# Performance work log

Hardware: AMD Instinct MI355X
Metric: run time of the kernel (lower is better)

The kernel has to match this reference:

```python
import jax, jax.numpy as jnp
import numpy as np

EPS = 1e-5

def _layernorm(x, gamma, beta):
    # normalize over last (channel) axis, per point
    mu = jnp.mean(x, axis=-1, keepdims=True)
    var = jnp.mean(jnp.square(x - mu), axis=-1, keepdims=True)
    return (x - mu) * jax.lax.rsqrt(var + EPS) * gamma + beta

def setup_inputs() -> dict:
    key = jax.random.key(0)
    ks = jax.random.split(key, 12)
    B, N, C, F = 32, 4096, 3, 1024
    points = jax.random.normal(ks[0], (B, N, C), dtype=jnp.float32)
    mask = jax.random.randint(ks[1], (B, 1, N), 0, 2, dtype=jnp.int32)
    s = 0.05
    return {
        "points": points,
        "mask": mask,
        "w1": jax.random.normal(ks[2], (128, C), dtype=jnp.float32) * s,      # conv1 (no bias)
        "g1": jnp.ones((128,), jnp.float32),                                   # norm1 gamma
        "be1": jnp.zeros((128,), jnp.float32),                                 # norm1 beta
        "w2": jax.random.normal(ks[3], (256, 128), dtype=jnp.float32) * s,     # conv2
        "b2": jax.random.normal(ks[4], (256,), dtype=jnp.float32) * s,
        "w3": jax.random.normal(ks[5], (512, 512), dtype=jnp.float32) * s,     # conv3 (no bias)
        "g2": jnp.ones((512,), jnp.float32),                                   # norm2 gamma
        "be2": jnp.zeros((512,), jnp.float32),                                 # norm2 beta
        "w4": jax.random.normal(ks[6], (F, 512), dtype=jnp.float32) * s,       # conv4
        "b4": jax.random.normal(ks[7], (F,), dtype=jnp.float32) * s,
    }

def reference(points, mask, w1, g1, be1, w2, b2, w3, g2, be2, w4, b4):
    # points: [B, N, C]; mask: [B, 1, N]
    vis = (mask[:, 0, :] != 0).astype(points.dtype)[..., None]  # [B, N, 1]
    # conv1 (1x1, no bias) as point-wise matmul
    h0 = jnp.einsum('bnc,kc->bnk', points, w1)                  # [B, N, 128]
    # masked LayerNorm: LN is per-point over channels, so compute densely and zero invisible points
    h1 = _layernorm(h0, g1, be1) * vis
    h2 = jax.nn.relu(h1)
    h3 = jnp.einsum('bnk,ok->bno', h2, w2) + b2                 # [B, N, 256]
    gmax = jnp.max(h3, axis=1, keepdims=True)                   # [B, 1, 256]
    dist = jnp.concatenate([jnp.broadcast_to(gmax, h3.shape), h3], axis=-1)  # [B, N, 512]
    h4 = jnp.einsum('bno,po->bnp', dist, w3)                    # [B, N, 512]
    h5 = _layernorm(h4, g2, be2) * vis
    h6 = jax.nn.relu(h5)
    h7 = jnp.einsum('bnp,fp->bnf', h6, w4) + b4                 # [B, N, F]
    return jnp.max(h7, axis=1)                                  # [B, F]
```

## Files before the change

kernel.cpp:

```cpp
#include <hip/hip_runtime.h>
#include <stdint.h>

#define LN_EPS 1e-5f

static __device__ __forceinline__ unsigned short f2bf_bits(float f) {
  union { float f; unsigned u; } v; v.f = f;
  unsigned r = v.u + 0x7FFFu + ((v.u >> 16) & 1u);
  return (unsigned short)(r >> 16);
}
static __device__ __forceinline__ float bf2f(unsigned short h) {
  union { unsigned u; float f; } v; v.u = ((unsigned)h) << 16;
  return v.f;
}

typedef __bf16 bf16x8 __attribute__((ext_vector_type(8)));
typedef float floatx4 __attribute__((ext_vector_type(4)));

typedef __attribute__((address_space(1))) unsigned int* gas_ptr;
typedef __attribute__((address_space(3))) unsigned int* las_ptr;
static __device__ __forceinline__ void async_cp16(const void* g, void* l) {
  __builtin_amdgcn_global_load_lds((gas_ptr)g, (las_ptr)l, 16, 0, 0);
}

__global__ __launch_bounds__(256) void perm_kernel(
    const int* __restrict__ mask, int* __restrict__ newrow, int* __restrict__ cnt) {
  const int b = blockIdx.x, t = threadIdx.x;
  const int base = b * 4096 + t * 16;
  int v[16]; int s = 0;
#pragma unroll
  for (int i = 0; i < 16; ++i) { v[i] = (mask[base + i] != 0); s += v[i]; }
  const int lane = t & 63, wv = t >> 6;
  int scan = s;
  for (int o = 1; o < 64; o <<= 1) { int x = __shfl_up(scan, o); if (lane >= o) scan += x; }
  __shared__ int wsum[4], woff[4], stotal;
  if (lane == 63) wsum[wv] = scan;
  __syncthreads();
  if (t == 0) { int a = 0; for (int k = 0; k < 4; ++k) { woff[k] = a; a += wsum[k]; } stotal = a; cnt[b] = a; }
  __syncthreads();
  const int excl = scan - s + woff[wv];
  const int total = stotal;
  int run = 0;
#pragma unroll
  for (int i = 0; i < 16; ++i) {
    const int pos = t * 16 + i;
    const int visBefore = excl + run;
    newrow[b * 4096 + pos] = v[i] ? visBefore : total + (pos - visBefore);
    run += v[i];
  }
}

__global__ __launch_bounds__(256) void conv1_ln_kernel(
    const float* __restrict__ points,
    const float* __restrict__ w1, const float* __restrict__ g1,
    const float* __restrict__ be1, unsigned short* __restrict__ h2,
    const int* __restrict__ newrow, const int* __restrict__ cnt,
    const float* __restrict__ w2, const float* __restrict__ b2,
    const float* __restrict__ w3, const float* __restrict__ w4,
    unsigned short* __restrict__ w2b, unsigned short* __restrict__ w4b,
    unsigned short* __restrict__ w23b, float* __restrict__ vecb) {
  if (blockIdx.x >= 32768) {
    const int bb = blockIdx.x - 32768;
    if (bb < 2176) {
      int idx = bb * 256 + threadIdx.x;
      if (idx < 32768) w2b[idx] = f2bf_bits(w2[idx]);
      else w4b[idx - 32768] = f2bf_bits(w4[idx - 32768]);
    } else {
      const int tid = threadIdx.x;
      const int p = (bb - 2176) * 2 + (tid >> 7);
      const int c = tid & 127;
      const float* w3r = w3 + (size_t)p * 512 + 256;
      float s = 0.f;
      for (int k = 0; k < 256; ++k) s += w3r[k] * w2[k * 128 + c];
      w23b[p * 128 + c] = f2bf_bits(s);
      if (c == 0) {
        float vb = 0.f;
        for (int k = 0; k < 256; ++k) vb += w3r[k] * b2[k];
        vecb[p] = vb;
      }
    }
    return;
  }
  const int lane = threadIdx.x & 63;
  const int wv = threadIdx.x >> 6;
  const size_t p = (size_t)blockIdx.x * 4 + wv;
  const int dest = newrow[p];
  const int cntb = cnt[p >> 12];
  const int ceilv = (cntb + 127) & ~127;
  if (dest >= ceilv) return;
  const bool vis = (dest < cntb);
  const float x0 = points[p * 3 + 0];
  const float x1 = points[p * 3 + 1];
  const float x2 = points[p * 3 + 2];
  const int c0 = lane * 2, c1 = c0 + 1;
  float h00 = w1[c0 * 3] * x0 + w1[c0 * 3 + 1] * x1 + w1[c0 * 3 + 2] * x2;
  float h01 = w1[c1 * 3] * x0 + w1[c1 * 3 + 1] * x1 + w1[c1 * 3 + 2] * x2;
  float s = h00 + h01;
  for (int o = 32; o; o >>= 1) s += __shfl_xor(s, o);
  const float mu = s * (1.f / 128.f);
  const float d0 = h00 - mu, d1 = h01 - mu;
  float q = d0 * d0 + d1 * d1;
  for (int o = 32; o; o >>= 1) q += __shfl_xor(q, o);
  const float rs = rsqrtf(q * (1.f / 128.f) + LN_EPS);
  const float y0 = vis ? fmaxf(d0 * rs * g1[c0] + be1[c0], 0.f) : 0.f;
  const float y1 = vis ? fmaxf(d1 * rs * g1[c1] + be1[c1], 0.f) : 0.f;
  union { unsigned u; unsigned short s2[2]; } pk;
  pk.s2[0] = f2bf_bits(y0);
  pk.s2[1] = f2bf_bits(y1);
  const size_t prow = (p & ~(size_t)4095) + (size_t)dest;
  ((unsigned*)h2)[prow * 64 + lane] = pk.u;
}

__global__ __launch_bounds__(256) void gemm23_fused(
    const unsigned short* __restrict__ A,
    const unsigned short* __restrict__ w2b, const unsigned short* __restrict__ w23b,
    unsigned short* __restrict__ h46, float* __restrict__ pg,
    const float* __restrict__ b2, const float* __restrict__ vecb,
    const int* __restrict__ cnt, int M) {
  __shared__ __align__(16) char smA[2][128 * 64];
  __shared__ __align__(16) char smB[2][128 * 64];
  __shared__ float lmax[2][128];

  const int tid = threadIdx.x;
  const int lane = tid & 63;
  const int w = tid >> 6;
  const int wm = w >> 1, wn = w & 1;

  const int gid = blockIdx.x;
  const int xcd = gid & 7;
  const int slot = gid >> 3;
  const int rowsPerXcd = (M >> 7) >> 3;
  const int rowTile = xcd * rowsPerXcd + slot / 6;
  const int colTile = slot % 6;
  const bool isPG = (colTile < 2);
  const int colBase = isPG ? colTile * 128 : (colTile - 2) * 128;
  const size_t rowBase = (size_t)rowTile * 128;
  const unsigned short* Bw = isPG ? w2b : w23b;

  const int cntb = cnt[rowBase >> 12];
  const int rb = (int)(rowBase & 4095);
  if (rb >= cntb) {
    if (isPG) {
      if (tid < 128) pg[(size_t)rowTile * 256 + colBase + tid] = b2[colBase + tid];
    }
    return;
  }

  floatx4 acc[4][4];
  const floatx4 zero = {0.f, 0.f, 0.f, 0.f};
#pragma unroll
  for (int i = 0; i < 4; ++i)
#pragma unroll
    for (int j = 0; j < 4; ++j) acc[i][j] = zero;

  const int rSub = lane >> 2;
  const int cb16 = (lane & 3) * 16;
  const size_t Kb = 256;
  const char* gA = (const char*)A + (rowBase + (size_t)(w * 32 + rSub)) * Kb + cb16;
  const char* gB = (const char*)Bw + ((size_t)colBase + (size_t)(w * 32 + rSub)) * Kb + cb16;
  char* lA0 = smA[0] + w * 2048;
  char* lA1 = smA[1] + w * 2048;
  char* lB0 = smB[0] + w * 2048;
  char* lB1 = smB[1] + w * 2048;
  const size_t skip16 = 16 * Kb;

  const int fm = lane & 15, fq = lane >> 4;
  const int fOff = fm * 64 + fq * 16;
  const char* pa0 = smA[0] + wm * 64 * 64 + fOff;
  const char* pa1 = smA[1] + wm * 64 * 64 + fOff;
  const char* pb0 = smB[0] + wn * 64 * 64 + fOff;
  const char* pb1 = smB[1] + wn * 64 * 64 + fOff;

  for (int k0 = 0; k0 < 128; k0 += 64) {
    async_cp16(gA, lA0);
    async_cp16(gA + skip16, lA0 + 1024);
    async_cp16(gA + 64, lA1);
    async_cp16(gA + 64 + skip16, lA1 + 1024);
    async_cp16(gB, lB0);
    async_cp16(gB + skip16, lB0 + 1024);
    async_cp16(gB + 64, lB1);
    async_cp16(gB + 64 + skip16, lB1 + 1024);
    gA += 128; gB += 128;
    __syncthreads();
    bf16x8 af0[4], bg0[4], af1[4], bg1[4];
#pragma unroll
    for (int i = 0; i < 4; ++i) af0[i] = *(const bf16x8*)(pa0 + i * 16 * 64);
#pragma unroll
    for (int j = 0; j < 4; ++j) bg0[j] = *(const bf16x8*)(pb0 + j * 16 * 64);
#pragma unroll
    for (int i = 0; i < 4; ++i)
#pragma unroll
      for (int j = 0; j < 4; ++j)
        acc[i][j] = __builtin_amdgcn_mfma_f32_16x16x32_bf16(af0[i], bg0[j], acc[i][j], 0, 0, 0);
#pragma unroll
    for (int i = 0; i < 4; ++i) af1[i] = *(const bf16x8*)(pa1 + i * 16 * 64);
#pragma unroll
    for (int j = 0; j < 4; ++j) bg1[j] = *(const bf16x8*)(pb1 + j * 16 * 64);
#pragma unroll
    for (int i = 0; i < 4; ++i)
#pragma unroll
      for (int j = 0; j < 4; ++j)
        acc[i][j] = __builtin_amdgcn_mfma_f32_16x16x32_bf16(af1[i], bg1[j], acc[i][j], 0, 0, 0);
    __syncthreads();
  }

  if (isPG) {
    float m4[4] = {-1e30f, -1e30f, -1e30f, -1e30f};
#pragma unroll
    for (int j = 0; j < 4; ++j) {
      const float ex = b2[colBase + wn * 64 + j * 16 + fm];
#pragma unroll
      for (int i = 0; i < 4; ++i)
#pragma unroll
        for (int r = 0; r < 4; ++r) m4[j] = fmaxf(m4[j], acc[i][j][r] + ex);
      m4[j] = fmaxf(m4[j], __shfl_xor(m4[j], 16));
      m4[j] = fmaxf(m4[j], __shfl_xor(m4[j], 32));
    }
    const float sel = (fq == 0) ? m4[0] : (fq == 1) ? m4[1] : (fq == 2) ? m4[2] : m4[3];
    lmax[wm][wn * 64 + fq * 16 + fm] = sel;
    __syncthreads();
    if (tid < 128) {
      const float v = fmaxf(lmax[0][tid], lmax[1][tid]);
      pg[(size_t)rowTile * 256 + colBase + tid] = v;
    }
  } else {
#pragma unroll
    for (int j = 0; j < 4; ++j) {
      const int col = colBase + wn * 64 + j * 16 + fm;
      const float ex = vecb[col];
#pragma unroll
      for (int i = 0; i < 4; ++i) {
        const size_t row0 = rowBase + wm * 64 + i * 16 + fq * 4;
#pragma unroll
        for (int r = 0; r < 4; ++r) {
          h46[(row0 + r) * 512 + col] = f2bf_bits(acc[i][j][r] + ex);
        }
      }
    }
  }
}

#define G4_BAR() __builtin_amdgcn_s_barrier()
#define G4_LGKM0() asm volatile("s_waitcnt lgkmcnt(0)" ::: "memory")
#define G4_LGKM8() asm volatile("s_waitcnt lgkmcnt(8)" ::: "memory")
#define G4_VM2() asm volatile("s_waitcnt vmcnt(2)" ::: "memory")
#define G4_VM0() asm volatile("s_waitcnt vmcnt(0)" ::: "memory")
#define G4_PRIO1() __builtin_amdgcn_s_setprio(1)
#define G4_PRIO0() __builtin_amdgcn_s_setprio(0)

#define G4_STG(bufi, h4, kt) do { \
  const char* _s = (((h4) < 2) ? srcA : srcB) + (size_t)((h4) & 1) * (128 * 1024) + (size_t)(kt) * 128; \
  char* _d = stDst + (bufi) * 65536 + ((h4) >> 1) * 32768 + ((h4) & 1) * 16384; \
  async_cp16(_s, _d); \
  async_cp16(_s + 64 * 1024, _d + 8192); \
} while (0)

#define G4_LDA(bufi, mh) do { \
  const char* _p = rdA + (bufi) * 65536 + (mh) * 8192; \
  af[0][0] = *(const bf16x8*)(_p + c0);        af[0][1] = *(const bf16x8*)(_p + c1); \
  af[1][0] = *(const bf16x8*)(_p + 2048 + c0); af[1][1] = *(const bf16x8*)(_p + 2048 + c1); \
  af[2][0] = *(const bf16x8*)(_p + 4096 + c0); af[2][1] = *(const bf16x8*)(_p + 4096 + c1); \
  af[3][0] = *(const bf16x8*)(_p + 6144 + c0); af[3][1] = *(const bf16x8*)(_p + 6144 + c1); \
} while (0)

#define G4_LDB(bufi, nh, bgx) do { \
  const char* _p = rdB + (bufi) * 65536 + (nh) * 4096; \
  bgx[0][0] = *(const bf16x8*)(_p + c0);        bgx[0][1] = *(const bf16x8*)(_p + c1); \
  bgx[1][0] = *(const bf16x8*)(_p + 2048 + c0); bgx[1][1] = *(const bf16x8*)(_p + 2048 + c1); \
} while (0)

#define G4_QUAD(mh, nh, bgx) do { \
  _Pragma("unroll") \
  for (int _m = 0; _m < 4; ++_m) { \
    _Pragma("unroll") \
    for (int _n = 0; _n < 2; ++_n) { \
      acc[(mh) * 4 + _m][(nh) * 2 + _n] = __builtin_amdgcn_mfma_f32_16x16x32_bf16( \
          af[_m][0], bgx[_n][0], acc[(mh) * 4 + _m][(nh) * 2 + _n], 0, 0, 0); \
      acc[(mh) * 4 + _m][(nh) * 2 + _n] = __builtin_amdgcn_mfma_f32_16x16x32_bf16( \
          af[_m][1], bgx[_n][1], acc[(mh) * 4 + _m][(nh) * 2 + _n], 0, 0, 0); \
    } \
  } \
} while (0)

__global__ __launch_bounds__(512, 2) void gemm4_8ph(
    const unsigned short* __restrict__ A, const unsigned short* __restrict__ Bw,
    float* __restrict__ outp2, const int* __restrict__ cnt) {
  extern __shared__ char sm[];

  const int tid = threadIdx.x;
  const int lane = tid & 63;
  const int w = tid >> 6;
  const int wm = w >> 2, wn = w & 3;

  const int gid = blockIdx.x;
  const int xcd = gid & 7;
  const int slot = gid >> 3;
  const int rowTile = xcd * 64 + (slot >> 2);
  const int colTile = slot & 3;
  const size_t rowBase = (size_t)rowTile * 256;
  const int colBase = colTile * 256;

  const int cntb = cnt[rowBase >> 12];
  const int rb = (int)(rowBase & 4095);
  if (rb >= cntb) {
    if (tid < 256) outp2[(size_t)rowTile * 1024 + colBase + tid] = 0.f;
    return;
  }

  const int rr = tid >> 3;
  const int csw = ((tid & 7) ^ (rr & 7)) << 4;
  const char* srcA = (const char*)A + (rowBase + (size_t)rr) * 1024 + csw;
  const char* srcB = (const char*)Bw + ((size_t)colBase + (size_t)rr) * 1024 + csw;
  char* stDst = sm + w * 1024;

  const int fr = lane & 15, fq = lane >> 4;
  const int c0 = (fq * 16) ^ ((lane & 7) << 4);
  const int c1 = ((fq * 16) | 64) ^ ((lane & 7) << 4);
  const char* rdA = sm + (wm * 128 + fr) * 128;
  const char* rdB = sm + 32768 + (wn * 64 + fr) * 128;

  floatx4 acc[8][4];
  const floatx4 zero = {0.f, 0.f, 0.f, 0.f};
#pragma unroll
  for (int i = 0; i < 8; ++i)
#pragma unroll
    for (int j = 0; j < 4; ++j) acc[i][j] = zero;

  bf16x8 af[4][2], bg0[2][2], bg1[2][2];

  G4_STG(0, 0, 0); G4_STG(0, 1, 0); G4_STG(0, 2, 0); G4_STG(0, 3, 0);
  G4_STG(1, 0, 1);
  G4_VM2(); G4_BAR();

  for (int it = 0; it < 3; ++it) {
    const int tO = 2 * it + 1, tE2 = 2 * it + 2, tO2 = 2 * it + 3;
    G4_LDA(0, 0); G4_LDB(0, 0, bg0); G4_STG(1, 1, tO); G4_LGKM8(); G4_BAR(); G4_LGKM0();
    G4_PRIO1(); G4_QUAD(0, 0, bg0); G4_PRIO0(); G4_BAR();
    G4_LDB(0, 1, bg1); G4_STG(1, 2, tO); G4_BAR(); G4_LGKM0();
    G4_PRIO1(); G4_QUAD(0, 1, bg1); G4_PRIO0(); G4_BAR();
    G4_LDA(0, 1); G4_STG(1, 3, tO); G4_BAR(); G4_LGKM0();
    G4_PRIO1(); G4_QUAD(1, 1, bg1); G4_PRIO0(); G4_BAR();
    G4_STG(0, 0, tE2); G4_VM2(); G4_BAR();
    G4_PRIO1(); G4_QUAD(1, 0, bg0); G4_PRIO0(); G4_BAR();
    G4_LDA(1, 0); G4_LDB(1, 0, bg0); G4_STG(0, 1, tE2); G4_LGKM8(); G4_BAR(); G4_LGKM0();
    G4_PRIO1(); G4_QUAD(0, 0, bg0); G4_PRIO0(); G4_BAR();
    G4_LDB(1, 1, bg1); G4_STG(0, 2, tE2); G4_BAR(); G4_LGKM0();
    G4_PRIO1(); G4_QUAD(0, 1, bg1); G4_PRIO0(); G4_BAR();
    G4_LDA(1, 1); G4_STG(0, 3, tE2); G4_BAR(); G4_LGKM0();
    G4_PRIO1(); G4_QUAD(1, 1, bg1); G4_PRIO0(); G4_BAR();
    G4_STG(1, 0, tO2); G4_VM2(); G4_BAR();
    G4_PRIO1(); G4_QUAD(1, 0, bg0); G4_PRIO0(); G4_BAR();
  }

  G4_LDA(0, 0); G4_LDB(0, 0, bg0); G4_STG(1, 1, 7); G4_LGKM8(); G4_BAR(); G4_LGKM0();
  G4_PRIO1(); G4_QUAD(0, 0, bg0); G4_PRIO0(); G4_BAR();
  G4_LDB(0, 1, bg1); G4_STG(1, 2, 7); G4_BAR(); G4_LGKM0();
  G4_PRIO1(); G4_QUAD(0, 1, bg1); G4_PRIO0(); G4_BAR();
  G4_LDA(0, 1); G4_STG(1, 3, 7); G4_BAR(); G4_LGKM0();
  G4_PRIO1(); G4_QUAD(1, 1, bg1); G4_PRIO0(); G4_BAR();
  G4_VM0(); G4_BAR();
  G4_PRIO1(); G4_QUAD(1, 0, bg0); G4_PRIO0(); G4_BAR();
  G4_LDA(1, 0); G4_LDB(1, 0, bg0); G4_BAR(); G4_LGKM0();
  G4_PRIO1(); G4_QUAD(0, 0, bg0); G4_PRIO0(); G4_BAR();
  G4_LDB(1, 1, bg1); G4_BAR(); G4_LGKM0();
  G4_PRIO1(); G4_QUAD(0, 1, bg1); G4_PRIO0(); G4_BAR();
  G4_LDA(1, 1); G4_BAR(); G4_LGKM0();
  G4_PRIO1(); G4_QUAD(1, 1, bg1); G4_PRIO0(); G4_BAR();
  G4_PRIO1(); G4_QUAD(1, 0, bg0); G4_PRIO0(); G4_BAR();

  float* smf = (float*)sm;
  float mv[4];
#pragma unroll
  for (int nj = 0; nj < 4; ++nj) {
    float m = -1e30f;
#pragma unroll
    for (int mi = 0; mi < 8; ++mi)
#pragma unroll
      for (int r = 0; r < 4; ++r) m = fmaxf(m, acc[mi][nj][r]);
    m = fmaxf(m, __shfl_xor(m, 16));
    m = fmaxf(m, __shfl_xor(m, 32));
    mv[nj] = m;
  }
  const float sel = (fq == 0) ? mv[0] : (fq == 1) ? mv[1] : (fq == 2) ? mv[2] : mv[3];
  smf[wm * 256 + wn * 64 + fq * 16 + fr] = sel;
  __syncthreads();
  if (tid < 256) {
    outp2[(size_t)rowTile * 1024 + colBase + tid] = fmaxf(smf[tid], smf[256 + tid]);
  }
}

__global__ __launch_bounds__(256) void gmax_cvec_kernel(
    const float* __restrict__ pg, const float* __restrict__ w3,
    float* __restrict__ cvec) {
  __shared__ float gm[256];
  const int b = blockIdx.x >> 2, quarter = blockIdx.x & 3;
  const int t = threadIdx.x;
  float m = -1e30f;
  for (int s = 0; s < 32; ++s) m = fmaxf(m, pg[((size_t)b * 32 + s) * 256 + t]);
  gm[t] = m;
  __syncthreads();
  const int lane = t & 63, wv = t >> 6;
  const float g0 = gm[lane * 4 + 0];
  const float g1 = gm[lane * 4 + 1];
  const float g2v = gm[lane * 4 + 2];
  const float g3 = gm[lane * 4 + 3];
  for (int pp = 0; pp < 32; ++pp) {
    const int p = quarter * 128 + wv * 32 + pp;
    const float4 wr = *(const float4*)(w3 + (size_t)p * 512 + lane * 4);
    float s = wr.x * g0 + wr.y * g1 + wr.z * g2v + wr.w * g3;
    for (int o = 32; o; o >>= 1) s += __shfl_xor(s, o);
    if (lane == 0) cvec[b * 512 + p] = s;
  }
}

__global__ __launch_bounds__(256) void ln2_kernel(
    unsigned short* __restrict__ h46, const int* __restrict__ cnt,
    const float* __restrict__ cvec,
    const float* __restrict__ g2, const float* __restrict__ be2) {
  const int lane = threadIdx.x & 63;
  const int wv = threadIdx.x >> 6;
  const size_t p = (size_t)blockIdx.x * 4 + wv;
  const int cb = cnt[p >> 12];
  const int pin = (int)(p & 4095);
  const int ceilv = (cb + 255) & ~255;
  if (pin >= ceilv) return;
  unsigned short* row = h46 + p * 512;
  const int c0 = lane * 8;
  if (pin >= cb) {
    const uint4 z = {0, 0, 0, 0};
    *(uint4*)(row + c0) = z;
    return;
  }
  const int b = (int)(p >> 12);
  union { uint4 v; unsigned short s[8]; } in;
  in.v = *(const uint4*)(row + c0);
  float cv[8];
  *(float4*)(cv) = *(const float4*)(cvec + b * 512 + c0);
  *(float4*)(cv + 4) = *(const float4*)(cvec + b * 512 + c0 + 4);
  float f[8];
  float s = 0.f;
#pragma unroll
  for (int k = 0; k < 8; ++k) { f[k] = bf2f(in.s[k]) + cv[k]; s += f[k]; }
  for (int o = 32; o; o >>= 1) s += __shfl_xor(s, o);
  const float mu = s * (1.f / 512.f);
  float q = 0.f;
#pragma unroll
  for (int k = 0; k < 8; ++k) { const float d = f[k] - mu; q += d * d; }
  for (int o = 32; o; o >>= 1) q += __shfl_xor(q, o);
  const float rs = rsqrtf(q * (1.f / 512.f) + LN_EPS);
  union { uint4 v; unsigned short s[8]; } outv;
#pragma unroll
  for (int k = 0; k < 8; ++k) {
    const float y = fmaxf((f[k] - mu) * rs * g2[c0 + k] + be2[c0 + k], 0.f);
    outv.s[k] = f2bf_bits(y);
  }
  *(uint4*)(row + c0) = outv.v;
}

__global__ __launch_bounds__(256) void final_kernel(
    const float* __restrict__ pmax, const float* __restrict__ b4,
    float* __restrict__ out) {
  const int idx = blockIdx.x * 256 + threadIdx.x;
  const int b = idx >> 10, f = idx & 1023;
  float m = -1e30f;
  for (int r = 0; r < 16; ++r) m = fmaxf(m, pmax[((size_t)(b * 16 + r)) * 1024 + f]);
  out[idx] = m + b4[f];
}

extern "C" void kernel_launch(void* const* d_in, const int* in_sizes, int n_in,
                              void* d_out, int out_size, void* d_ws, size_t ws_size,
                              hipStream_t stream) {
  const float* points = (const float*)d_in[0];
  const int* mask = (const int*)d_in[1];
  const float* w1 = (const float*)d_in[2];
  const float* g1 = (const float*)d_in[3];
  const float* be1 = (const float*)d_in[4];
  const float* w2 = (const float*)d_in[5];
  const float* b2 = (const float*)d_in[6];
  const float* w3 = (const float*)d_in[7];
  const float* g2 = (const float*)d_in[8];
  const float* be2 = (const float*)d_in[9];
  const float* w4 = (const float*)d_in[10];
  const float* b4 = (const float*)d_in[11];
  float* out = (float*)d_out;
  char* ws = (char*)d_ws;

  const size_t OFF_H46 = 0;
  const size_t OFF_H2 = 134217728;
  const size_t OFF_W2B = OFF_H2 + 33554432;
  const size_t OFF_W4B = OFF_W2B + 65536;
  const size_t OFF_W23B = OFF_W4B + 1048576;
  const size_t OFF_VECB = OFF_W23B + 131072;
  const size_t OFF_PG = OFF_VECB + 2048;
  const size_t OFF_CVEC = OFF_PG + 1048576;
  const size_t OFF_PMAX = OFF_CVEC + 65536;
  const size_t OFF_CNT = OFF_PMAX + 4194304;
  const size_t OFF_NEWROW = OFF_CNT + 4096;

  unsigned short* h2 = (unsigned short*)(ws + OFF_H2);
  unsigned short* h46 = (unsigned short*)(ws + OFF_H46);
  unsigned short* w2b = (unsigned short*)(ws + OFF_W2B);
  unsigned short* w4b = (unsigned short*)(ws + OFF_W4B);
  unsigned short* w23b = (unsigned short*)(ws + OFF_W23B);
  float* vecb = (float*)(ws + OFF_VECB);
  float* pg = (float*)(ws + OFF_PG);
  float* cvecp = (float*)(ws + OFF_CVEC);
  float* pmaxp = (float*)(ws + OFF_PMAX);
  int* cntp = (int*)(ws + OFF_CNT);
  int* newrow = (int*)(ws + OFF_NEWROW);

  static bool s_attr_done = false;
  if (!s_attr_done) {
    hipFuncSetAttribute((const void*)gemm4_8ph,
                        hipFuncAttributeMaxDynamicSharedMemorySize, 131072);
    s_attr_done = true;
  }

  perm_kernel<<<32, 256, 0, stream>>>(mask, newrow, cntp);
  conv1_ln_kernel<<<32768 + 2176 + 256, 256, 0, stream>>>(
      points, w1, g1, be1, h2, newrow, cntp, w2, b2, w3, w4, w2b, w4b, w23b, vecb);
  gemm23_fused<<<6144, 256, 0, stream>>>(h2, w2b, w23b, h46, pg, b2, vecb, cntp, 131072);
  gmax_cvec_kernel<<<128, 256, 0, stream>>>(pg, w3, cvecp);
  ln2_kernel<<<32768, 256, 0, stream>>>(h46, cntp, cvecp, g2, be2);
  gemm4_8ph<<<2048, 512, 131072, stream>>>(h46, w4b, pmaxp, cntp);
  final_kernel<<<128, 256, 0, stream>>>(pmaxp, b4, out);
}
```

Baseline: 268.1 us.

## Compact tile work lists so GEMM and LN2 blocks map only to visible tiles

Adds a per-batch prefix scan over visible-point counts that builds compacted lists of occupied 128-row and 256-row tiles. gemm23, ln2 and gemm4 map block indices directly onto these lists, so the leading blocks all do real work and the surplus blocks exit at once. Before, empty tiles were spread across the grid and each wrote placeholder partial results. The reduction kernels now loop only over occupied tiles and seed their max with the empty-point value (b2 or zero) when a batch has invisible points. This removes wasted scheduling and placeholder writes, but drops the XCD-aware tile mapping, which may hurt L2 locality.

```diff
diff --git a/kernel.cpp b/kernel.cpp
--- a/kernel.cpp
+++ b/kernel.cpp
@@ -57,14 +57,16 @@
     const float* __restrict__ w2, const float* __restrict__ b2,
     const float* __restrict__ w3, const float* __restrict__ w4,
     unsigned short* __restrict__ w2b, unsigned short* __restrict__ w4b,
-    unsigned short* __restrict__ w23b, float* __restrict__ vecb) {
+    unsigned short* __restrict__ w23b, float* __restrict__ vecb,
+    int* __restrict__ hdr, unsigned short* __restrict__ tl128,
+    unsigned short* __restrict__ tl256) {
   if (blockIdx.x >= 32768) {
     const int bb = blockIdx.x - 32768;
     if (bb < 2176) {
       int idx = bb * 256 + threadIdx.x;
       if (idx < 32768) w2b[idx] = f2bf_bits(w2[idx]);
       else w4b[idx - 32768] = f2bf_bits(w4[idx - 32768]);
-    } else {
+    } else if (bb < 2176 + 256) {
       const int tid = threadIdx.x;
       const int p = (bb - 2176) * 2 + (tid >> 7);
       const int c = tid & 127;
@@ -76,6 +78,24 @@
         float vb = 0.f;
         for (int k = 0; k < 256; ++k) vb += w3r[k] * b2[k];
         vecb[p] = vb;
+      }
+    } else {
+      const int lane = threadIdx.x;
+      if (lane < 64) {
+        const int c = (lane < 32) ? cnt[lane] : 0;
+        const int n128 = (c + 127) >> 7;
+        const int n256 = (c + 255) >> 8;
+        int s128 = n128, s256 = n256;
+        for (int o = 1; o < 64; o <<= 1) {
+          int x = __shfl_up(s128, o); if (lane >= o) s128 += x;
+          int y = __shfl_up(s256, o); if (lane >= o) s256 += y;
+        }
+        if (lane == 31) { hdr[0] = s128; hdr[1] = s256; }
+        if (lane < 32) {
+          const int e128 = s128 - n128, e256 = s256 - n256;
+          for (int j = 0; j < n128; ++j) tl128[e128 + j] = (unsigned short)(lane * 32 + j);
+          for (int j = 0; j < n256; ++j) tl256[e256 + j] = (unsigned short)(lane * 16 + j);
+        }
       }
     }
     return;
@@ -115,35 +135,26 @@
     const unsigned short* __restrict__ w2b, const unsigned short* __restrict__ w23b,
     unsigned short* __restrict__ h46, float* __restrict__ pg,
     const float* __restrict__ b2, const float* __restrict__ vecb,
-    const int* __restrict__ cnt, int M) {
+    const int* __restrict__ hdr, const unsigned short* __restrict__ tl128) {
   __shared__ __align__(16) char smA[2][128 * 64];
   __shared__ __align__(16) char smB[2][128 * 64];
   __shared__ float lmax[2][128];
+
+  const int nW = hdr[0] * 6;
+  if (blockIdx.x >= nW) return;
+  const int t6 = blockIdx.x / 6;
+  const int colTile = blockIdx.x - t6 * 6;
+  const int rowTile = tl128[t6];
 
   const int tid = threadIdx.x;
   const int lane = tid & 63;
   const int w = tid >> 6;
   const int wm = w >> 1, wn = w & 1;
 
-  const int gid = blockIdx.x;
-  const int xcd = gid & 7;
-  const int slot = gid >> 3;
-  const int rowsPerXcd = (M >> 7) >> 3;
-  const int rowTile = xcd * rowsPerXcd + slot / 6;
-  const int colTile = slot % 6;
   const bool isPG = (colTile < 2);
   const int colBase = isPG ? colTile * 128 : (colTile - 2) * 128;
   const size_t rowBase = (size_t)rowTile * 128;
   const unsigned short* Bw = isPG ? w2b : w23b;
-
-  const int cntb = cnt[rowBase >> 12];
-  const int rb = (int)(rowBase & 4095);
-  if (rb >= cntb) {
-    if (isPG) {
-      if (tid < 128) pg[(size_t)rowTile * 256 + colBase + tid] = b2[colBase + tid];
-    }
-    return;
-  }
 
   floatx4 acc[4][4];
   const floatx4 zero = {0.f, 0.f, 0.f, 0.f};
@@ -283,28 +294,22 @@
 
 __global__ __launch_bounds__(512, 2) void gemm4_8ph(
     const unsigned short* __restrict__ A, const unsigned short* __restrict__ Bw,
-    float* __restrict__ outp2, const int* __restrict__ cnt) {
+    float* __restrict__ outp2, const int* __restrict__ hdr,
+    const unsigned short* __restrict__ tl256) {
   extern __shared__ char sm[];
+
+  const int nW = hdr[1] * 4;
+  if (blockIdx.x >= nW) return;
+  const int rowTile = tl256[blockIdx.x >> 2];
+  const int colTile = blockIdx.x & 3;
 
   const int tid = threadIdx.x;
   const int lane = tid & 63;
   const int w = tid >> 6;
   const int wm = w >> 2, wn = w & 3;
 
-  const int gid = blockIdx.x;
-  const int xcd = gid & 7;
-  const int slot = gid >> 3;
-  const int rowTile = xcd * 64 + (slot >> 2);
-  const int colTile = slot & 3;
   const size_t rowBase = (size_t)rowTile * 256;
   const int colBase = colTile * 256;
-
-  const int cntb = cnt[rowBase >> 12];
-  const int rb = (int)(rowBase & 4095);
-  if (rb >= cntb) {
-    if (tid < 256) outp2[(size_t)rowTile * 1024 + colBase + tid] = 0.f;
-    return;
-  }
 
   const int rr = tid >> 3;
   const int csw = ((tid & 7) ^ (rr & 7)) << 4;
@@ -390,12 +395,15 @@
 
 __global__ __launch_bounds__(256) void gmax_cvec_kernel(
     const float* __restrict__ pg, const float* __restrict__ w3,
-    float* __restrict__ cvec) {
+    float* __restrict__ cvec, const int* __restrict__ cnt,
+    const float* __restrict__ b2) {
   __shared__ float gm[256];
   const int b = blockIdx.x >> 2, quarter = blockIdx.x & 3;
   const int t = threadIdx.x;
-  float m = -1e30f;
-  for (int s = 0; s < 32; ++s) m = fmaxf(m, pg[((size_t)b * 32 + s) * 256 + t]);
+  const int c = cnt[b];
+  const int nt = (c + 127) >> 7;
+  float m = (c < 4096) ? b2[t] : -1e30f;
+  for (int s = 0; s < nt; ++s) m = fmaxf(m, pg[((size_t)b * 32 + s) * 256 + t]);
   gm[t] = m;
   __syncthreads();
   const int lane = t & 63, wv = t >> 6;
@@ -415,14 +423,17 @@
 __global__ __launch_bounds__(256) void ln2_kernel(
     unsigned short* __restrict__ h46, const int* __restrict__ cnt,
     const float* __restrict__ cvec,
-    const float* __restrict__ g2, const float* __restrict__ be2) {
+    const float* __restrict__ g2, const float* __restrict__ be2,
+    const int* __restrict__ hdr, const unsigned short* __restrict__ tl256) {
+  const int nW = hdr[1] * 64;
+  if (blockIdx.x >= nW) return;
+  const int rowTile = tl256[blockIdx.x >> 6];
   const int lane = threadIdx.x & 63;
   const int wv = threadIdx.x >> 6;
-  const size_t p = (size_t)blockIdx.x * 4 + wv;
-  const int cb = cnt[p >> 12];
+  const size_t p = (size_t)rowTile * 256 + ((blockIdx.x & 63) * 4 + wv);
+  const int b = rowTile >> 4;
+  const int cb = cnt[b];
   const int pin = (int)(p & 4095);
-  const int ceilv = (cb + 255) & ~255;
-  if (pin >= ceilv) return;
   unsigned short* row = h46 + p * 512;
   const int c0 = lane * 8;
   if (pin >= cb) {
@@ -430,7 +441,6 @@
     *(uint4*)(row + c0) = z;
     return;
   }
-  const int b = (int)(p >> 12);
   union { uint4 v; unsigned short s[8]; } in;
   in.v = *(const uint4*)(row + c0);
   float cv[8];
@@ -458,11 +468,13 @@
 
 __global__ __launch_bounds__(256) void final_kernel(
     const float* __restrict__ pmax, const float* __restrict__ b4,
-    float* __restrict__ out) {
+    float* __restrict__ out, const int* __restrict__ cnt) {
   const int idx = blockIdx.x * 256 + threadIdx.x;
   const int b = idx >> 10, f = idx & 1023;
-  float m = -1e30f;
-  for (int r = 0; r < 16; ++r) m = fmaxf(m, pmax[((size_t)(b * 16 + r)) * 1024 + f]);
+  const int c = cnt[b];
+  const int nt = (c + 255) >> 8;
+  float m = (c < 4096) ? 0.f : -1e30f;
+  for (int r = 0; r < nt; ++r) m = fmaxf(m, pmax[((size_t)(b * 16 + r)) * 1024 + f]);
   out[idx] = m + b4[f];
 }
 
@@ -495,6 +507,9 @@
   const size_t OFF_PMAX = OFF_CVEC + 65536;
   const size_t OFF_CNT = OFF_PMAX + 4194304;
   const size_t OFF_NEWROW = OFF_CNT + 4096;
+  const size_t OFF_HDR = OFF_NEWROW + 524288;
+  const size_t OFF_TL128 = OFF_HDR + 64;
+  const size_t OFF_TL256 = OFF_TL128 + 2048;
 
   unsigned short* h2 = (unsigned short*)(ws + OFF_H2);
   unsigned short* h46 = (unsigned short*)(ws + OFF_H46);
@@ -507,6 +522,9 @@
   float* pmaxp = (float*)(ws + OFF_PMAX);
   int* cntp = (int*)(ws + OFF_CNT);
   int* newrow = (int*)(ws + OFF_NEWROW);
+  int* hdr = (int*)(ws + OFF_HDR);
+  unsigned short* tl128 = (unsigned short*)(ws + OFF_TL128);
+  unsigned short* tl256 = (unsigned short*)(ws + OFF_TL256);
 
   static bool s_attr_done = false;
   if (!s_attr_done) {
@@ -516,11 +534,12 @@
   }
 
   perm_kernel<<<32, 256, 0, stream>>>(mask, newrow, cntp);
-  conv1_ln_kernel<<<32768 + 2176 + 256, 256, 0, stream>>>(
-      points, w1, g1, be1, h2, newrow, cntp, w2, b2, w3, w4, w2b, w4b, w23b, vecb);
-  gemm23_fused<<<6144, 256, 0, stream>>>(h2, w2b, w23b, h46, pg, b2, vecb, cntp, 131072);
-  gmax_cvec_kernel<<<128, 256, 0, stream>>>(pg, w3, cvecp);
-  ln2_kernel<<<32768, 256, 0, stream>>>(h46, cntp, cvecp, g2, be2);
-  gemm4_8ph<<<2048, 512, 131072, stream>>>(h46, w4b, pmaxp, cntp);
-  final_kernel<<<128, 256, 0, stream>>>(pmaxp, b4, out);
-}
+  conv1_ln_kernel<<<32768 + 2176 + 256 + 1, 256, 0, stream>>>(
+      points, w1, g1, be1, h2, newrow, cntp, w2, b2, w3, w4, w2b, w4b, w23b, vecb,
+      hdr, tl128, tl256);
+  gemm23_fused<<<6144, 256, 0, stream>>>(h2, w2b, w23b, h46, pg, b2, vecb, hdr, tl128);
+  gmax_cvec_kernel<<<128, 256, 0, stream>>>(pg, w3, cvecp, cntp, b2);
+  ln2_kernel<<<32768, 256, 0, stream>>>(h46, cntp, cvecp, g2, be2, hdr, tl256);
+  gemm4_8ph<<<2048, 512, 131072, stream>>>(h46, w4b, pmaxp, hdr, tl256);
+  final_kernel<<<128, 256, 0, stream>>>(pmaxp, b4, out, cntp);
+}
```

Result: slower. 284.6 us (+6.2%).

## Reuse A tile across two column tiles and skip empty-tile writes

Applied to the files above, without the earlier changes.

The fused GEMM2/GEMM23 kernel now loads each block's full 128x128 A tile into shared memory once and reuses it across two 128-column output phases, halving the grid and the A reloads. Fully masked row tiles now return early without writing placeholder values. The downstream reductions (gmax_cvec and final) read the valid count and iterate only over populated tiles, adding the bias or zero contribution for masked points analytically. In exchange, each block does twice the work, shared memory use grows, and correctness now depends on the count-based tile bounds matching the early-exit logic.

```diff
diff --git a/kernel.cpp b/kernel.cpp
--- a/kernel.cpp
+++ b/kernel.cpp
@@ -115,124 +115,125 @@
     const unsigned short* __restrict__ w2b, const unsigned short* __restrict__ w23b,
     unsigned short* __restrict__ h46, float* __restrict__ pg,
     const float* __restrict__ b2, const float* __restrict__ vecb,
-    const int* __restrict__ cnt, int M) {
-  __shared__ __align__(16) char smA[2][128 * 64];
+    const int* __restrict__ cnt) {
+  __shared__ __align__(16) char smA[4][128 * 64];
   __shared__ __align__(16) char smB[2][128 * 64];
   __shared__ float lmax[2][128];
+
+  const int gid = blockIdx.x;
+  const int xcd = gid & 7;
+  const int slot = gid >> 3;
+  const int rowTile = xcd * 128 + slot / 3;
+  const int pair = slot - (slot / 3) * 3;
+  const size_t rowBase = (size_t)rowTile * 128;
+
+  const int cntb = cnt[rowBase >> 12];
+  const int rb = (int)(rowBase & 4095);
+  if (rb >= cntb) return;
 
   const int tid = threadIdx.x;
   const int lane = tid & 63;
   const int w = tid >> 6;
   const int wm = w >> 1, wn = w & 1;
 
-  const int gid = blockIdx.x;
-  const int xcd = gid & 7;
-  const int slot = gid >> 3;
-  const int rowsPerXcd = (M >> 7) >> 3;
-  const int rowTile = xcd * rowsPerXcd + slot / 6;
-  const int colTile = slot % 6;
-  const bool isPG = (colTile < 2);
-  const int colBase = isPG ? colTile * 128 : (colTile - 2) * 128;
-  const size_t rowBase = (size_t)rowTile * 128;
+  const bool isPG = (pair == 0);
   const unsigned short* Bw = isPG ? w2b : w23b;
-
-  const int cntb = cnt[rowBase >> 12];
-  const int rb = (int)(rowBase & 4095);
-  if (rb >= cntb) {
-    if (isPG) {
-      if (tid < 128) pg[(size_t)rowTile * 256 + colBase + tid] = b2[colBase + tid];
-    }
-    return;
-  }
-
-  floatx4 acc[4][4];
-  const floatx4 zero = {0.f, 0.f, 0.f, 0.f};
-#pragma unroll
-  for (int i = 0; i < 4; ++i)
-#pragma unroll
-    for (int j = 0; j < 4; ++j) acc[i][j] = zero;
 
   const int rSub = lane >> 2;
   const int cb16 = (lane & 3) * 16;
-  const size_t Kb = 256;
-  const char* gA = (const char*)A + (rowBase + (size_t)(w * 32 + rSub)) * Kb + cb16;
-  const char* gB = (const char*)Bw + ((size_t)colBase + (size_t)(w * 32 + rSub)) * Kb + cb16;
-  char* lA0 = smA[0] + w * 2048;
-  char* lA1 = smA[1] + w * 2048;
+  const size_t skip16 = 16 * 256;
+
+  const char* gA = (const char*)A + (rowBase + (size_t)(w * 32 + rSub)) * 256 + cb16;
+#pragma unroll
+  for (int q = 0; q < 4; ++q) {
+    async_cp16(gA + q * 64, smA[q] + w * 2048);
+    async_cp16(gA + q * 64 + skip16, smA[q] + w * 2048 + 1024);
+  }
+
   char* lB0 = smB[0] + w * 2048;
   char* lB1 = smB[1] + w * 2048;
-  const size_t skip16 = 16 * Kb;
 
   const int fm = lane & 15, fq = lane >> 4;
   const int fOff = fm * 64 + fq * 16;
-  const char* pa0 = smA[0] + wm * 64 * 64 + fOff;
-  const char* pa1 = smA[1] + wm * 64 * 64 + fOff;
   const char* pb0 = smB[0] + wn * 64 * 64 + fOff;
   const char* pb1 = smB[1] + wn * 64 * 64 + fOff;
 
-  for (int k0 = 0; k0 < 128; k0 += 64) {
-    async_cp16(gA, lA0);
-    async_cp16(gA + skip16, lA0 + 1024);
-    async_cp16(gA + 64, lA1);
-    async_cp16(gA + 64 + skip16, lA1 + 1024);
-    async_cp16(gB, lB0);
-    async_cp16(gB + skip16, lB0 + 1024);
-    async_cp16(gB + 64, lB1);
-    async_cp16(gB + 64 + skip16, lB1 + 1024);
-    gA += 128; gB += 128;
-    __syncthreads();
-    bf16x8 af0[4], bg0[4], af1[4], bg1[4];
-#pragma unroll
-    for (int i = 0; i < 4; ++i) af0[i] = *(const bf16x8*)(pa0 + i * 16 * 64);
-#pragma unroll
-    for (int j = 0; j < 4; ++j) bg0[j] = *(const bf16x8*)(pb0 + j * 16 * 64);
+  const floatx4 zero = {0.f, 0.f, 0.f, 0.f};
+
+  for (int ph = 0; ph < 2; ++ph) {
+    const int bRow = isPG ? ph * 128 : ((pair - 1) * 256 + ph * 128);
+    floatx4 acc[4][4];
 #pragma unroll
     for (int i = 0; i < 4; ++i)
 #pragma unroll
-      for (int j = 0; j < 4; ++j)
-        acc[i][j] = __builtin_amdgcn_mfma_f32_16x16x32_bf16(af0[i], bg0[j], acc[i][j], 0, 0, 0);
-#pragma unroll
-    for (int i = 0; i < 4; ++i) af1[i] = *(const bf16x8*)(pa1 + i * 16 * 64);
-#pragma unroll
-    for (int j = 0; j < 4; ++j) bg1[j] = *(const bf16x8*)(pb1 + j * 16 * 64);
-#pragma unroll
-    for (int i = 0; i < 4; ++i)
-#pragma unroll
-      for (int j = 0; j < 4; ++j)
-        acc[i][j] = __builtin_amdgcn_mfma_f32_16x16x32_bf16(af1[i], bg1[j], acc[i][j], 0, 0, 0);
-    __syncthreads();
-  }
-
-  if (isPG) {
-    float m4[4] = {-1e30f, -1e30f, -1e30f, -1e30f};
-#pragma unroll
-    for (int j = 0; j < 4; ++j) {
-      const float ex = b2[colBase + wn * 64 + j * 16 + fm];
+      for (int j = 0; j < 4; ++j) acc[i][j] = zero;
+
+    const char* gB = (const char*)Bw + ((size_t)(bRow + w * 32 + rSub)) * 256 + cb16;
+
+    for (int k0i = 0; k0i < 2; ++k0i) {
+      async_cp16(gB, lB0);
+      async_cp16(gB + skip16, lB0 + 1024);
+      async_cp16(gB + 64, lB1);
+      async_cp16(gB + 64 + skip16, lB1 + 1024);
+      gB += 128;
+      __syncthreads();
+      const char* pa0 = smA[2 * k0i] + wm * 64 * 64 + fOff;
+      const char* pa1 = smA[2 * k0i + 1] + wm * 64 * 64 + fOff;
+      bf16x8 af0[4], bg0[4], af1[4], bg1[4];
+#pragma unroll
+      for (int i = 0; i < 4; ++i) af0[i] = *(const bf16x8*)(pa0 + i * 16 * 64);
+#pragma unroll
+      for (int j = 0; j < 4; ++j) bg0[j] = *(const bf16x8*)(pb0 + j * 16 * 64);
 #pragma unroll
       for (int i = 0; i < 4; ++i)
 #pragma unroll
-        for (int r = 0; r < 4; ++r) m4[j] = fmaxf(m4[j], acc[i][j][r] + ex);
-      m4[j] = fmaxf(m4[j], __shfl_xor(m4[j], 16));
-      m4[j] = fmaxf(m4[j], __shfl_xor(m4[j], 32));
+        for (int j = 0; j < 4; ++j)
+          acc[i][j] = __builtin_amdgcn_mfma_f32_16x16x32_bf16(af0[i], bg0[j], acc[i][j], 0, 0, 0);
+#pragma unroll
+      for (int i = 0; i < 4; ++i) af1[i] = *(const bf16x8*)(pa1 + i * 16 * 64);
+#pragma unroll
+      for (int j = 0; j < 4; ++j) bg1[j] = *(const bf16x8*)(pb1 + j * 16 * 64);
+#pragma unroll
+      for (int i = 0; i < 4; ++i)
+#pragma unroll
+        for (int j = 0; j < 4; ++j)
+          acc[i][j] = __builtin_amdgcn_mfma_f32_16x16x32_bf16(af1[i], bg1[j], acc[i][j], 0, 0, 0);
+      __syncthreads();
     }
-    const float sel = (fq == 0) ? m4[0] : (fq == 1) ? m4[1] : (fq == 2) ? m4[2] : m4[3];
-    lmax[wm][wn * 64 + fq * 16 + fm] = sel;
-    __syncthreads();
-    if (tid < 128) {
-      const float v = fmaxf(lmax[0][tid], lmax[1][tid]);
-      pg[(size_t)rowTile * 256 + colBase + tid] = v;
-    }
-  } else {
-#pragma unroll
-    for (int j = 0; j < 4; ++j) {
-      const int col = colBase + wn * 64 + j * 16 + fm;
-      const float ex = vecb[col];
-#pragma unroll
-      for (int i = 0; i < 4; ++i) {
-        const size_t row0 = rowBase + wm * 64 + i * 16 + fq * 4;
-#pragma unroll
-        for (int r = 0; r < 4; ++r) {
-          h46[(row0 + r) * 512 + col] = f2bf_bits(acc[i][j][r] + ex);
+
+    if (isPG) {
+      const int colBase = ph * 128;
+      float m4[4] = {-1e30f, -1e30f, -1e30f, -1e30f};
+#pragma unroll
+      for (int j = 0; j < 4; ++j) {
+        const float ex = b2[colBase + wn * 64 + j * 16 + fm];
+#pragma unroll
+        for (int i = 0; i < 4; ++i)
+#pragma unroll
+          for (int r = 0; r < 4; ++r) m4[j] = fmaxf(m4[j], acc[i][j][r] + ex);
+        m4[j] = fmaxf(m4[j], __shfl_xor(m4[j], 16));
+        m4[j] = fmaxf(m4[j], __shfl_xor(m4[j], 32));
+      }
+      const float sel = (fq == 0) ? m4[0] : (fq == 1) ? m4[1] : (fq == 2) ? m4[2] : m4[3];
+      lmax[wm][wn * 64 + fq * 16 + fm] = sel;
+      __syncthreads();
+      if (tid < 128) {
+        const float v = fmaxf(lmax[0][tid], lmax[1][tid]);
+        pg[(size_t)rowTile * 256 + colBase + tid] = v;
+      }
+    } else {
+      const int colBase = (pair - 1) * 256 + ph * 128;
+#pragma unroll
+      for (int j = 0; j < 4; ++j) {
+        const int col = colBase + wn * 64 + j * 16 + fm;
+        const float ex = vecb[col];
+#pragma unroll
+        for (int i = 0; i < 4; ++i) {
+          const size_t row0 = rowBase + wm * 64 + i * 16 + fq * 4;
+#pragma unroll
+          for (int r = 0; r < 4; ++r) {
+            h46[(row0 + r) * 512 + col] = f2bf_bits(acc[i][j][r] + ex);
+          }
         }
       }
     }
@@ -286,11 +287,6 @@
     float* __restrict__ outp2, const int* __restrict__ cnt) {
   extern __shared__ char sm[];
 
-  const int tid = threadIdx.x;
-  const int lane = tid & 63;
-  const int w = tid >> 6;
-  const int wm = w >> 2, wn = w & 3;
-
   const int gid = blockIdx.x;
   const int xcd = gid & 7;
   const int slot = gid >> 3;
@@ -301,10 +297,12 @@
 
   const int cntb = cnt[rowBase >> 12];
   const int rb = (int)(rowBase & 4095);
-  if (rb >= cntb) {
-    if (tid < 256) outp2[(size_t)rowTile * 1024 + colBase + tid] = 0.f;
-    return;
-  }
+  if (rb >= cntb) return;
+
+  const int tid = threadIdx.x;
+  const int lane = tid & 63;
+  const int w = tid >> 6;
+  const int wm = w >> 2, wn = w & 3;
 
   const int rr = tid >> 3;
   const int csw = ((tid & 7) ^ (rr & 7)) << 4;
@@ -390,12 +388,15 @@
 
 __global__ __launch_bounds__(256) void gmax_cvec_kernel(
     const float* __restrict__ pg, const float* __restrict__ w3,
-    float* __restrict__ cvec) {
+    float* __restrict__ cvec, const int* __restrict__ cnt,
+    const float* __restrict__ b2) {
   __shared__ float gm[256];
   const int b = blockIdx.x >> 2, quarter = blockIdx.x & 3;
   const int t = threadIdx.x;
-  float m = -1e30f;
-  for (int s = 0; s < 32; ++s) m = fmaxf(m, pg[((size_t)b * 32 + s) * 256 + t]);
+  const int c = cnt[b];
+  const int nt = (c + 127) >> 7;
+  float m = (c < 4096) ? b2[t] : -1e30f;
+  for (int s = 0; s < nt; ++s) m = fmaxf(m, pg[((size_t)b * 32 + s) * 256 + t]);
   gm[t] = m;
   __syncthreads();
   const int lane = t & 63, wv = t >> 6;
@@ -458,11 +459,13 @@
 
 __global__ __launch_bounds__(256) void final_kernel(
     const float* __restrict__ pmax, const float* __restrict__ b4,
-    float* __restrict__ out) {
+    float* __restrict__ out, const int* __restrict__ cnt) {
   const int idx = blockIdx.x * 256 + threadIdx.x;
   const int b = idx >> 10, f = idx & 1023;
-  float m = -1e30f;
-  for (int r = 0; r < 16; ++r) m = fmaxf(m, pmax[((size_t)(b * 16 + r)) * 1024 + f]);
+  const int c = cnt[b];
+  const int nt = (c + 255) >> 8;
+  float m = (c < 4096) ? 0.f : -1e30f;
+  for (int r = 0; r < nt; ++r) m = fmaxf(m, pmax[((size_t)(b * 16 + r)) * 1024 + f]);
   out[idx] = m + b4[f];
 }
 
@@ -518,9 +521,9 @@
   perm_kernel<<<32, 256, 0, stream>>>(mask, newrow, cntp);
   conv1_ln_kernel<<<32768 + 2176 + 256, 256, 0, stream>>>(
       points, w1, g1, be1, h2, newrow, cntp, w2, b2, w3, w4, w2b, w4b, w23b, vecb);
-  gemm23_fused<<<6144, 256, 0, stream>>>(h2, w2b, w23b, h46, pg, b2, vecb, cntp, 131072);
-  gmax_cvec_kernel<<<128, 256, 0, stream>>>(pg, w3, cvecp);
+  gemm23_fused<<<3072, 256, 0, stream>>>(h2, w2b, w23b, h46, pg, b2, vecb, cntp);
+  gmax_cvec_kernel<<<128, 256, 0, stream>>>(pg, w3, cvecp, cntp, b2);
   ln2_kernel<<<32768, 256, 0, stream>>>(h46, cntp, cvecp, g2, be2);
   gemm4_8ph<<<2048, 512, 131072, stream>>>(h46, w4b, pmaxp, cntp);
-  final_kernel<<<128, 256, 0, stream>>>(pmaxp, b4, out);
-}
+  final_kernel<<<128, 256, 0, stream>>>(pmaxp, b4, out, cntp);
+}
```

After: 270.6 us. No clear change (+0.9%).
